# Optimization experiments

Hardware: AMD Instinct MI355X
Metric: run time of the kernel (lower is better)

Reference implementation:

```python
import jax, jax.numpy as jnp
import numpy as np

CONTEXT = 3  # config['context']
B, H, W = 8, 256, 256
NBR = 2 * CONTEXT  # number of similarity branches


def _conv(x, w, b):
    # x: [N, Cin, H, W], w: [Cout, Cin, kh, kw], SAME padding, stride 1
    y = jax.lax.conv_general_dilated(x, w, (1, 1), 'SAME',
                                     dimension_numbers=('NCHW', 'OIHW', 'NCHW'))
    return y + b[None, :, None, None]


def setup_inputs() -> dict:
    key = jax.random.key(0)
    ks = jax.random.split(key, 5)
    x = jax.random.normal(ks[0], (B, 2 * CONTEXT + 1, H, W), dtype=jnp.float32)
    # kaiming-ish scaled inits
    W1 = jax.random.normal(ks[1], (NBR, 64, 2, 3, 3), dtype=jnp.float32) * (2.0 / (64 * 9)) ** 0.5
    b1 = jnp.zeros((NBR, 64), dtype=jnp.float32)
    W2 = jax.random.normal(ks[2], (NBR, 1, 64, 1, 1), dtype=jnp.float32) * (2.0 / 1) ** 0.5 * 0.1
    b2 = jnp.zeros((NBR, 1), dtype=jnp.float32)
    Wm = jax.random.normal(ks[3], (7, 7, 3, 3), dtype=jnp.float32) * (2.0 / (7 * 9)) ** 0.5
    bm = jnp.zeros((7,), dtype=jnp.float32)
    return {'x': x, 'W1': W1, 'b1': b1, 'W2': W2, 'b2': b2, 'Wm': Wm, 'bm': bm}


def reference(x, W1, b1, W2, b2, Wm, bm):
    # mode == 'context' path just returns x; this implements the main path.
    base = x[:, CONTEXT:CONTEXT + 1]                                  # [B,1,H,W]
    checks = jnp.concatenate([x[:, :CONTEXT], x[:, CONTEXT + 1:]], axis=1)  # [B,6,H,W]
    check_e = checks[:, :, None]                                      # [B,6,1,H,W]
    base_e = jnp.broadcast_to(base[:, None], check_e.shape)           # [B,6,1,H,W]
    # channel order: pre-frames -> (base, check); post-frames -> (check, base)
    ch0 = jnp.concatenate([base_e[:, :CONTEXT], check_e[:, CONTEXT:]], axis=2 - 2 + 2)  # placeholder
    ch0 = jnp.concatenate([base_e[:, :CONTEXT], check_e[:, CONTEXT:]], axis=1)
    ch1 = jnp.concatenate([check_e[:, :CONTEXT], base_e[:, CONTEXT:]], axis=1)
    pairs = jnp.concatenate([ch0, ch1], axis=2)                       # [B,6,2,H,W]
    pairs = jnp.swapaxes(pairs, 0, 1)                                 # [6,B,2,H,W]

    def branch(pair, w1, bb1, w2, bb2):
        h = jax.nn.relu(_conv(pair, w1, bb1))                         # [B,64,H,W]
        return jax.nn.sigmoid(_conv(h, w2, bb2))                      # [B,1,H,W]

    sims = jax.vmap(branch)(pairs, W1, b1, W2, b2)                    # [6,B,1,H,W]
    weighted = sims[:, :, 0] * jnp.swapaxes(checks, 0, 1)             # [6,B,H,W]
    weighted = jnp.swapaxes(weighted, 0, 1)                           # [B,6,H,W]
    combined = jnp.concatenate([weighted[:, :CONTEXT], base, weighted[:, CONTEXT:]], axis=1)  # [B,7,H,W]
    return _conv(combined, Wm, bm)                                    # [B,7,H,W]
```

## Files before the change

kernel.cpp:

```cpp
#include <hip/hip_runtime.h>
#include <math.h>

#define Bn 8
#define Hn 256
#define Wn 256
#define HW (Hn * Wn)
#define ROWS 4
#define RP 264
#define ZW (12 * RP)

typedef __attribute__((ext_vector_type(8))) short bf16x8;
typedef __attribute__((ext_vector_type(4))) float f32x4;

__device__ __forceinline__ unsigned int pk_bits(unsigned int lo,
                                                unsigned int hi) {
  return __builtin_amdgcn_perm(hi, lo, 0x07060302u);
}
__device__ __forceinline__ unsigned int pk_bf16(float lo, float hi) {
  return pk_bits(__float_as_uint(lo), __float_as_uint(hi));
}

__device__ __constant__ const int T0c[8] = {0, 1, 2, 9, 10, 11, 3, 4};
__device__ __constant__ const int T1c[8] = {6, 7, 8, 15, 16, 17, 12, 13};
__device__ __constant__ const int T2c[8] = {5, 14, -1, -1, -1, -1, -1, -1};

__global__ __launch_bounds__(256) void sim_kernel(
    const float* __restrict__ x,
    const float* __restrict__ W1,
    const float* __restrict__ b1,
    const float* __restrict__ W2,
    const float* __restrict__ b2,
    float* __restrict__ comb)
{
  __shared__ float rowsF[12 * RP + 64];
  __shared__ uint4 wq[4][64];

  int bi = blockIdx.x;
  int n  = bi >> 9;
  int b  = (bi >> 6) & 7;
  int h0 = (bi & 63) * ROWS;
  int cc = (n < 3) ? n : n + 1;
  int t = threadIdx.x;

  const float* xb     = x + (size_t)b * 7 * HW;
  const float* basep  = xb + 3 * HW;
  const float* checkp = xb + (size_t)cc * HW;

  {
    int f = t >> 6, qq = (t >> 4) & 3, m = t & 15;
    int bsrc = (n < 3) ? 0 : 1;
    const float* wch = W1 + ((size_t)(n * 64 + 16 * f + m)) * 18;
    unsigned int kv[4];
#pragma unroll
    for (int jj = 0; jj < 4; ++jj) {
      int ja = 2 * jj, jb = 2 * jj + 1;
      int ta = (qq == 0) ? T0c[ja] : (qq == 1) ? T1c[ja]
               : (qq == 2) ? T2c[ja] : -1;
      int tb = (qq == 0) ? T0c[jb] : (qq == 1) ? T1c[jb]
               : (qq == 2) ? T2c[jb] : -1;
      float va = 0.f, vb = 0.f;
      if (ta >= 0) {
        int pl = ta / 9, rem = ta - pl * 9;
        va = wch[(pl ? 1 - bsrc : bsrc) * 9 + rem];
      }
      if (tb >= 0) {
        int pl = tb / 9, rem = tb - pl * 9;
        vb = wch[(pl ? 1 - bsrc : bsrc) * 9 + rem];
      }
      kv[jj] = pk_bf16(va, vb);
    }
    wq[f][(qq << 4) + m] = make_uint4(kv[0], kv[1], kv[2], kv[3]);
  }

  int lane = t & 63, wvid = t >> 6;
  int q = lane >> 4, m_ = lane & 15;
  float w2v[4][4];
  f32x4 b1vv[4];
#pragma unroll
  for (int f = 0; f < 4; ++f) {
    float4 tw = *(const float4*)&W2[n * 64 + 16 * f + 4 * q];
    float4 tb = *(const float4*)&b1[n * 64 + 16 * f + 4 * q];
    w2v[f][0] = tw.x; w2v[f][1] = tw.y; w2v[f][2] = tw.z; w2v[f][3] = tw.w;
    b1vv[f][0] = tb.x; b1vv[f][1] = tb.y;
    b1vv[f][2] = tb.z; b1vv[f][3] = tb.w;
  }
  float bb = b2[n];

  {
    int col = (t & 63) << 2;
#pragma unroll
    for (int it = 0; it < 3; ++it) {
      int rf = it * 4 + (t >> 6);
      int pl = (rf >= 6) ? 1 : 0;
      int j  = rf - pl * 6;
      int hh = h0 - 1 + j;
      const float* src = pl ? checkp : basep;
      float4 val = make_float4(0.f, 0.f, 0.f, 0.f);
      if ((unsigned)hh < (unsigned)Hn)
        val = *(const float4*)(src + hh * Wn + col);
      *(float4*)&rowsF[rf * RP + 4 + col] = val;
    }
    if (t < 12) {
      rowsF[t * RP + 3] = 0.f;
      rowsF[t * RP + 260] = 0.f;
    }
    if (t >= 192) rowsF[ZW + (t - 192)] = 0.f;
  }

  const unsigned int* rowsU = (const unsigned int*)rowsF;
  unsigned int addr[8], vbit[8];
#pragma unroll
  for (int jh = 0; jh < 8; ++jh) {
    int tap = (q == 0) ? T0c[jh] : (q == 1) ? T1c[jh]
              : (q == 2) ? T2c[jh] : -1;
    if (tap >= 0) {
      int pl = tap / 9, rem = tap - pl * 9;
      int rr = rem / 3, dx = rem - rr * 3;
      addr[jh] = (pl * 6 + rr) * RP + 3 + dx + wvid * 64 + m_;
      vbit[jh] = 1u;
    } else {
      addr[jh] = (unsigned)ZW;
      vbit[jh] = 0u;
    }
  }

  __syncthreads();

  bf16x8 afrag[4];
#pragma unroll
  for (int f = 0; f < 4; ++f) afrag[f] = *(const bf16x8*)&wq[f][lane];

  float* combcc = comb + ((size_t)b * 7 + cc) * HW;
  float* comb3  = comb + ((size_t)b * 7 + 3) * HW;
  int pxs = wvid * 64 + lane;

#pragma unroll 1
  for (int r = 0; r < ROWS; ++r) {
    int h = h0 + r;
    unsigned int rowoff = (unsigned)(r * RP);

    unsigned int base[8];
#pragma unroll
    for (int jh = 0; jh < 8; ++jh) base[jh] = addr[jh] + vbit[jh] * rowoff;

    float g[4];
#pragma unroll
    for (int half = 0; half < 2; ++half) {
      unsigned int dlo[8], dhi[8];
#pragma unroll
      for (int jh = 0; jh < 8; ++jh) {
        dlo[jh] = rowsU[base[jh] + half * 32];
        dhi[jh] = rowsU[base[jh] + half * 32 + 16];
      }
#pragma unroll
      for (int j = 0; j < 2; ++j) {
        const unsigned int* d = j ? dhi : dlo;
        union { unsigned int u[4]; bf16x8 v; } bu;
#pragma unroll
        for (int jj = 0; jj < 4; ++jj)
          bu.u[jj] = pk_bits(d[2 * jj], d[2 * jj + 1]);

        f32x4 acc[4];
#pragma unroll
        for (int f = 0; f < 4; ++f)
          acc[f] = __builtin_amdgcn_mfma_f32_16x16x32_bf16(afrag[f], bu.v,
                                                           b1vv[f], 0, 0, 0);

        float spA = 0.f, spB = 0.f;
#pragma unroll
        for (int rr = 0; rr < 4; ++rr) {
          spA = fmaf(w2v[0][rr], fmaxf(acc[0][rr], 0.f), spA);
          spB = fmaf(w2v[2][rr], fmaxf(acc[2][rr], 0.f), spB);
          spA = fmaf(w2v[1][rr], fmaxf(acc[1][rr], 0.f), spA);
          spB = fmaf(w2v[3][rr], fmaxf(acc[3][rr], 0.f), spB);
        }
        float sp = spA + spB;
        sp += __shfl_xor(sp, 16, 64);
        sp += __shfl_xor(sp, 32, 64);
        sp += bb;

        float e = __builtin_amdgcn_exp2f(sp * -1.442695041f);
        g[2 * half + j] = __builtin_amdgcn_rcpf(1.f + e);
      }
    }

    int hi = lane >> 4;
    float gsel = (hi == 0) ? g[0] : (hi == 1) ? g[1] : (hi == 2) ? g[2] : g[3];
    float ccv = rowsF[(6 + r + 1) * RP + 4 + pxs];
    combcc[h * Wn + pxs] = gsel * ccv;
    if (n == 0) comb3[h * Wn + pxs] = rowsF[(r + 1) * RP + 4 + pxs];
  }
}

__global__ __launch_bounds__(256) void mix_kernel(
    const float* __restrict__ comb,
    const float* __restrict__ Wm,
    const float* __restrict__ bm,
    float* __restrict__ out)
{
  __shared__ float mr[28 * RP];

  int bi = blockIdx.x;
  int b  = bi >> 7;
  int h0 = (bi & 127) << 1;
  int t = threadIdx.x;

  for (int u = t; u < 28 * 64; u += 256) {
    int rf = u >> 6;
    int col = (u & 63) << 2;
    int ic = rf >> 2, j = rf & 3;
    int hh = h0 - 1 + j;
    float4 v = make_float4(0.f, 0.f, 0.f, 0.f);
    if ((unsigned)hh < (unsigned)Hn)
      v = *(const float4*)(comb + ((size_t)b * 7 + ic) * HW + hh * Wn + col);
    *(float4*)&mr[rf * RP + 4 + col] = v;
  }
  if (t < 28) {
    mr[t * RP + 3] = 0.f;
    mr[t * RP + 260] = 0.f;
  }
  __syncthreads();

  int r   = t >> 7;
  int px0 = (t & 127) << 1;
  int h   = h0 + r;

  float acc[7][2];
#pragma unroll
  for (int oc = 0; oc < 7; ++oc) {
    float bv = bm[oc];
    acc[oc][0] = bv;
    acc[oc][1] = bv;
  }

#pragma unroll 1
  for (int ic = 0; ic < 7; ++ic) {
    float w[3][4];
#pragma unroll
    for (int dy = 0; dy < 3; ++dy) {
      const float* rp = &mr[(ic * 4 + r + dy) * RP + 3 + px0];
      w[dy][0] = rp[0]; w[dy][1] = rp[1];
      w[dy][2] = rp[2]; w[dy][3] = rp[3];
    }
    const float* wp = Wm + ic * 9;
#pragma unroll
    for (int oc = 0; oc < 7; ++oc) {
      const float* wo = wp + oc * 63;
#pragma unroll
      for (int dy = 0; dy < 3; ++dy)
#pragma unroll
        for (int dx = 0; dx < 3; ++dx) {
          float wvv = wo[dy * 3 + dx];
          acc[oc][0] = fmaf(wvv, w[dy][0 + dx], acc[oc][0]);
          acc[oc][1] = fmaf(wvv, w[dy][1 + dx], acc[oc][1]);
        }
    }
  }

  float* ob = out + (size_t)b * 7 * HW + h * Wn + px0;
#pragma unroll
  for (int oc = 0; oc < 7; ++oc)
    *(float2*)(ob + (size_t)oc * HW) = make_float2(acc[oc][0], acc[oc][1]);
}

extern "C" void kernel_launch(void* const* d_in, const int* in_sizes, int n_in,
                              void* d_out, int out_size, void* d_ws, size_t ws_size,
                              hipStream_t stream) {
  const float* x  = (const float*)d_in[0];
  const float* W1 = (const float*)d_in[1];
  const float* b1 = (const float*)d_in[2];
  const float* W2 = (const float*)d_in[3];
  const float* b2 = (const float*)d_in[4];
  const float* Wm = (const float*)d_in[5];
  const float* bm = (const float*)d_in[6];
  float* out  = (float*)d_out;
  float* comb = (float*)d_ws;

  sim_kernel<<<6 * 8 * (Hn / ROWS), 256, 0, stream>>>(x, W1, b1, W2, b2, comb);
  mix_kernel<<<8 * (Hn / 2), 256, 0, stream>>>(comb, Wm, bm, out);
}
```

Measured before the change: 120.9 us.

## Switch sim conv to 32x32x16 MFMA with split tap groups

Recasts the first-layer 3x3 conv GEMM from 16x16x32 bf16 MFMAs to 32x32x16 bf16 MFMAs. Each half-wave now covers one of the two input planes with 8 taps, and a second zero-padded MFMA handles the two leftover taps. The weight fragment layout, bias and W2 register layout, LDS addressing and the reduction all change to match. This removes the tap lookup tables and the zero-row trick, and it needs fewer cross-lane shuffles. In exchange it issues extra mostly-zero MFMAs and uses more accumulator registers.

```diff
diff --git a/kernel.cpp b/kernel.cpp
--- a/kernel.cpp
+++ b/kernel.cpp
@@ -7,10 +7,9 @@
 #define HW (Hn * Wn)
 #define ROWS 4
 #define RP 264
-#define ZW (12 * RP)
 
 typedef __attribute__((ext_vector_type(8))) short bf16x8;
-typedef __attribute__((ext_vector_type(4))) float f32x4;
+typedef __attribute__((ext_vector_type(16))) float f32x16;
 
 __device__ __forceinline__ unsigned int pk_bits(unsigned int lo,
                                                 unsigned int hi) {
@@ -20,9 +19,10 @@
   return pk_bits(__float_as_uint(lo), __float_as_uint(hi));
 }
 
-__device__ __constant__ const int T0c[8] = {0, 1, 2, 9, 10, 11, 3, 4};
-__device__ __constant__ const int T1c[8] = {6, 7, 8, 15, 16, 17, 12, 13};
-__device__ __constant__ const int T2c[8] = {5, 14, -1, -1, -1, -1, -1, -1};
+__device__ __forceinline__ void pos2rrdx(int pos, int& rr, int& dx) {
+  rr = (pos < 3) ? 0 : (pos < 6) ? 1 : 2;
+  dx = pos - rr * 3;
+}
 
 __global__ __launch_bounds__(256) void sim_kernel(
     const float* __restrict__ x,
@@ -32,8 +32,9 @@
     const float* __restrict__ b2,
     float* __restrict__ comb)
 {
-  __shared__ float rowsF[12 * RP + 64];
-  __shared__ uint4 wq[4][64];
+  __shared__ float rowsF[12 * RP];
+  __shared__ uint4 wq1[2][64];
+  __shared__ uint4 wq2[2][64];
 
   int bi = blockIdx.x;
   int n  = bi >> 9;
@@ -47,43 +48,49 @@
   const float* checkp = xb + (size_t)cc * HW;
 
   {
-    int f = t >> 6, qq = (t >> 4) & 3, m = t & 15;
+    int g  = (t >> 6) & 1;
+    int l  = t & 63;
+    int ch = 32 * g + (l & 31);
+    int kh = l >> 5;
     int bsrc = (n < 3) ? 0 : 1;
-    const float* wch = W1 + ((size_t)(n * 64 + 16 * f + m)) * 18;
-    unsigned int kv[4];
-#pragma unroll
-    for (int jj = 0; jj < 4; ++jj) {
-      int ja = 2 * jj, jb = 2 * jj + 1;
-      int ta = (qq == 0) ? T0c[ja] : (qq == 1) ? T1c[ja]
-               : (qq == 2) ? T2c[ja] : -1;
-      int tb = (qq == 0) ? T0c[jb] : (qq == 1) ? T1c[jb]
-               : (qq == 2) ? T2c[jb] : -1;
-      float va = 0.f, vb = 0.f;
-      if (ta >= 0) {
-        int pl = ta / 9, rem = ta - pl * 9;
-        va = wch[(pl ? 1 - bsrc : bsrc) * 9 + rem];
+    const float* wch = W1 + ((size_t)(n * 64 + ch)) * 18;
+    int src = kh ? (1 - bsrc) : bsrc;
+    if (t < 128) {
+      unsigned int kv[4];
+#pragma unroll
+      for (int jj = 0; jj < 4; ++jj) {
+        int r0, d0, r1, d1;
+        pos2rrdx(2 * jj, r0, d0);
+        pos2rrdx(2 * jj + 1, r1, d1);
+        kv[jj] = pk_bf16(wch[src * 9 + r0 * 3 + d0],
+                         wch[src * 9 + r1 * 3 + d1]);
       }
-      if (tb >= 0) {
-        int pl = tb / 9, rem = tb - pl * 9;
-        vb = wch[(pl ? 1 - bsrc : bsrc) * 9 + rem];
-      }
-      kv[jj] = pk_bf16(va, vb);
-    }
-    wq[f][(qq << 4) + m] = make_uint4(kv[0], kv[1], kv[2], kv[3]);
+      wq1[g][l] = make_uint4(kv[0], kv[1], kv[2], kv[3]);
+    } else {
+      unsigned int k0 = 0u;
+      if (kh == 0)
+        k0 = pk_bf16(wch[bsrc * 9 + 8], wch[(1 - bsrc) * 9 + 8]);
+      wq2[g][l] = make_uint4(k0, 0u, 0u, 0u);
+    }
   }
 
   int lane = t & 63, wvid = t >> 6;
-  int q = lane >> 4, m_ = lane & 15;
-  float w2v[4][4];
-  f32x4 b1vv[4];
-#pragma unroll
-  for (int f = 0; f < 4; ++f) {
-    float4 tw = *(const float4*)&W2[n * 64 + 16 * f + 4 * q];
-    float4 tb = *(const float4*)&b1[n * 64 + 16 * f + 4 * q];
-    w2v[f][0] = tw.x; w2v[f][1] = tw.y; w2v[f][2] = tw.z; w2v[f][3] = tw.w;
-    b1vv[f][0] = tb.x; b1vv[f][1] = tb.y;
-    b1vv[f][2] = tb.z; b1vv[f][3] = tb.w;
-  }
+  int kh = lane >> 5, ln5 = lane & 31;
+
+  f32x16 b1c[2];
+  float w2v[2][16];
+#pragma unroll
+  for (int g = 0; g < 2; ++g)
+#pragma unroll
+    for (int blk = 0; blk < 4; ++blk) {
+      int o = n * 64 + 32 * g + 8 * blk + 4 * kh;
+      float4 tb = *(const float4*)&b1[o];
+      float4 tw = *(const float4*)&W2[o];
+      b1c[g][4 * blk + 0] = tb.x; b1c[g][4 * blk + 1] = tb.y;
+      b1c[g][4 * blk + 2] = tb.z; b1c[g][4 * blk + 3] = tb.w;
+      w2v[g][4 * blk + 0] = tw.x; w2v[g][4 * blk + 1] = tw.y;
+      w2v[g][4 * blk + 2] = tw.z; w2v[g][4 * blk + 3] = tw.w;
+    }
   float bb = b2[n];
 
   {
@@ -104,31 +111,24 @@
       rowsF[t * RP + 3] = 0.f;
       rowsF[t * RP + 260] = 0.f;
     }
-    if (t >= 192) rowsF[ZW + (t - 192)] = 0.f;
   }
 
   const unsigned int* rowsU = (const unsigned int*)rowsF;
-  unsigned int addr[8], vbit[8];
-#pragma unroll
-  for (int jh = 0; jh < 8; ++jh) {
-    int tap = (q == 0) ? T0c[jh] : (q == 1) ? T1c[jh]
-              : (q == 2) ? T2c[jh] : -1;
-    if (tap >= 0) {
-      int pl = tap / 9, rem = tap - pl * 9;
-      int rr = rem / 3, dx = rem - rr * 3;
-      addr[jh] = (pl * 6 + rr) * RP + 3 + dx + wvid * 64 + m_;
-      vbit[jh] = 1u;
-    } else {
-      addr[jh] = (unsigned)ZW;
-      vbit[jh] = 0u;
-    }
-  }
+  int pxb = 64 * wvid + ln5;
+  unsigned int b0 = (kh * 6 + 0) * RP + 3 + pxb;
+  unsigned int b1a = (kh * 6 + 1) * RP + 3 + pxb;
+  unsigned int b2a = (kh * 6 + 2) * RP + 3 + pxb;
+  unsigned int bt16 = (0 * 6 + 2) * RP + 3 + 2 + pxb;
+  unsigned int bt17 = (1 * 6 + 2) * RP + 3 + 2 + pxb;
 
   __syncthreads();
 
-  bf16x8 afrag[4];
-#pragma unroll
-  for (int f = 0; f < 4; ++f) afrag[f] = *(const bf16x8*)&wq[f][lane];
+  bf16x8 af1[2], af2[2];
+#pragma unroll
+  for (int g = 0; g < 2; ++g) {
+    af1[g] = *(const bf16x8*)&wq1[g][lane];
+    af2[g] = *(const bf16x8*)&wq2[g][lane];
+  }
 
   float* combcc = comb + ((size_t)b * 7 + cc) * HW;
   float* comb3  = comb + ((size_t)b * 7 + 3) * HW;
@@ -137,55 +137,62 @@
 #pragma unroll 1
   for (int r = 0; r < ROWS; ++r) {
     int h = h0 + r;
-    unsigned int rowoff = (unsigned)(r * RP);
-
-    unsigned int base[8];
-#pragma unroll
-    for (int jh = 0; jh < 8; ++jh) base[jh] = addr[jh] + vbit[jh] * rowoff;
-
-    float g[4];
-#pragma unroll
-    for (int half = 0; half < 2; ++half) {
-      unsigned int dlo[8], dhi[8];
-#pragma unroll
-      for (int jh = 0; jh < 8; ++jh) {
-        dlo[jh] = rowsU[base[jh] + half * 32];
-        dhi[jh] = rowsU[base[jh] + half * 32 + 16];
+
+    float gg[2];
+#pragma unroll
+    for (int s = 0; s < 2; ++s) {
+      unsigned int off = (unsigned)(r * RP + 32 * s);
+
+      unsigned int d0 = rowsU[b0 + off];
+      unsigned int d1 = rowsU[b0 + off + 1];
+      unsigned int d2 = rowsU[b0 + off + 2];
+      unsigned int d3 = rowsU[b1a + off];
+      unsigned int d4 = rowsU[b1a + off + 1];
+      unsigned int d5 = rowsU[b1a + off + 2];
+      unsigned int d6 = rowsU[b2a + off];
+      unsigned int d7 = rowsU[b2a + off + 1];
+      union { unsigned int u[4]; bf16x8 v; } bu;
+      bu.u[0] = pk_bits(d0, d1);
+      bu.u[1] = pk_bits(d2, d3);
+      bu.u[2] = pk_bits(d4, d5);
+      bu.u[3] = pk_bits(d6, d7);
+
+      unsigned int e0 = rowsU[bt16 + off];
+      unsigned int e1 = rowsU[bt17 + off];
+      union { unsigned int u[4]; bf16x8 v; } b2u;
+      b2u.u[0] = kh ? 0u : pk_bits(e0, e1);
+      b2u.u[1] = 0u; b2u.u[2] = 0u; b2u.u[3] = 0u;
+
+      f32x16 acc0 = __builtin_amdgcn_mfma_f32_32x32x16_bf16(af1[0], bu.v,
+                                                            b1c[0], 0, 0, 0);
+      acc0 = __builtin_amdgcn_mfma_f32_32x32x16_bf16(af2[0], b2u.v,
+                                                     acc0, 0, 0, 0);
+      f32x16 acc1 = __builtin_amdgcn_mfma_f32_32x32x16_bf16(af1[1], bu.v,
+                                                            b1c[1], 0, 0, 0);
+      acc1 = __builtin_amdgcn_mfma_f32_32x32x16_bf16(af2[1], b2u.v,
+                                                     acc1, 0, 0, 0);
+
+      float s0 = 0.f, s1 = 0.f, s2 = 0.f, s3 = 0.f;
+#pragma unroll
+      for (int i = 0; i < 4; ++i) {
+        s0 = fmaf(w2v[0][i],      fmaxf(acc0[i], 0.f),      s0);
+        s1 = fmaf(w2v[0][4 + i],  fmaxf(acc0[4 + i], 0.f),  s1);
+        s2 = fmaf(w2v[0][8 + i],  fmaxf(acc0[8 + i], 0.f),  s2);
+        s3 = fmaf(w2v[0][12 + i], fmaxf(acc0[12 + i], 0.f), s3);
+        s0 = fmaf(w2v[1][i],      fmaxf(acc1[i], 0.f),      s0);
+        s1 = fmaf(w2v[1][4 + i],  fmaxf(acc1[4 + i], 0.f),  s1);
+        s2 = fmaf(w2v[1][8 + i],  fmaxf(acc1[8 + i], 0.f),  s2);
+        s3 = fmaf(w2v[1][12 + i], fmaxf(acc1[12 + i], 0.f), s3);
       }
-#pragma unroll
-      for (int j = 0; j < 2; ++j) {
-        const unsigned int* d = j ? dhi : dlo;
-        union { unsigned int u[4]; bf16x8 v; } bu;
-#pragma unroll
-        for (int jj = 0; jj < 4; ++jj)
-          bu.u[jj] = pk_bits(d[2 * jj], d[2 * jj + 1]);
-
-        f32x4 acc[4];
-#pragma unroll
-        for (int f = 0; f < 4; ++f)
-          acc[f] = __builtin_amdgcn_mfma_f32_16x16x32_bf16(afrag[f], bu.v,
-                                                           b1vv[f], 0, 0, 0);
-
-        float spA = 0.f, spB = 0.f;
-#pragma unroll
-        for (int rr = 0; rr < 4; ++rr) {
-          spA = fmaf(w2v[0][rr], fmaxf(acc[0][rr], 0.f), spA);
-          spB = fmaf(w2v[2][rr], fmaxf(acc[2][rr], 0.f), spB);
-          spA = fmaf(w2v[1][rr], fmaxf(acc[1][rr], 0.f), spA);
-          spB = fmaf(w2v[3][rr], fmaxf(acc[3][rr], 0.f), spB);
-        }
-        float sp = spA + spB;
-        sp += __shfl_xor(sp, 16, 64);
-        sp += __shfl_xor(sp, 32, 64);
-        sp += bb;
-
-        float e = __builtin_amdgcn_exp2f(sp * -1.442695041f);
-        g[2 * half + j] = __builtin_amdgcn_rcpf(1.f + e);
-      }
-    }
-
-    int hi = lane >> 4;
-    float gsel = (hi == 0) ? g[0] : (hi == 1) ? g[1] : (hi == 2) ? g[2] : g[3];
+      float sp = (s0 + s1) + (s2 + s3);
+      sp += __shfl_xor(sp, 32, 64);
+      sp += bb;
+
+      float e = __builtin_amdgcn_exp2f(sp * -1.442695041f);
+      gg[s] = __builtin_amdgcn_rcpf(1.f + e);
+    }
+
+    float gsel = kh ? gg[1] : gg[0];
     float ccv = rowsF[(6 + r + 1) * RP + 4 + pxs];
     combcc[h * Wn + pxs] = gsel * ccv;
     if (n == 0) comb3[h * Wn + pxs] = rowsF[(r + 1) * RP + 4 + pxs];
```

After: 126.0 us. 1.04x slower.
